# Kernel tuning notes

Measured on AMD Instinct MI355X. Metric: run time of the kernel, lower is better.

## Reference

```python
import jax, jax.numpy as jnp
import numpy as np

D_MODEL = 1024
HEADS = 16
D_K = D_MODEL // HEADS
D_FF = 4096
B, S = 4, 2048
EPS = 1e-5


def _layer_norm(x, gamma, beta):
    mu = jnp.mean(x, axis=-1, keepdims=True)
    var = jnp.mean(jnp.square(x - mu), axis=-1, keepdims=True)
    return (x - mu) * jax.lax.rsqrt(var + EPS) * gamma + beta


def setup_inputs() -> dict:
    key = jax.random.key(0)
    ks = jax.random.split(key, 16)
    s_in = 1.0 / np.sqrt(D_MODEL)
    s_ff = 1.0 / np.sqrt(D_FF)
    inp = {
        "x": jax.random.normal(ks[0], (B, S, D_MODEL), dtype=jnp.float32),
        "src_mask": jnp.ones((B, 1, 1, S), dtype=jnp.int32),
        "Wq": jax.random.uniform(ks[1], (D_MODEL, D_MODEL), jnp.float32, -s_in, s_in),
        "bq": jnp.zeros((D_MODEL,), jnp.float32),
        "Wk": jax.random.uniform(ks[2], (D_MODEL, D_MODEL), jnp.float32, -s_in, s_in),
        "bk": jnp.zeros((D_MODEL,), jnp.float32),
        "Wv": jax.random.uniform(ks[3], (D_MODEL, D_MODEL), jnp.float32, -s_in, s_in),
        "bv": jnp.zeros((D_MODEL,), jnp.float32),
        "Wo": jax.random.uniform(ks[4], (D_MODEL, D_MODEL), jnp.float32, -s_in, s_in),
        "bo": jnp.zeros((D_MODEL,), jnp.float32),
        "W1": jax.random.uniform(ks[5], (D_MODEL, D_FF), jnp.float32, -s_in, s_in),
        "b1": jnp.zeros((D_FF,), jnp.float32),
        "W2": jax.random.uniform(ks[6], (D_FF, D_MODEL), jnp.float32, -s_ff, s_ff),
        "b2": jnp.zeros((D_MODEL,), jnp.float32),
        "g1": jnp.ones((D_MODEL,), jnp.float32),
        "be1": jnp.zeros((D_MODEL,), jnp.float32),
        "g2": jnp.ones((D_MODEL,), jnp.float32),
        "be2": jnp.zeros((D_MODEL,), jnp.float32),
    }
    return inp


def reference(x, src_mask, Wq, bq, Wk, bk, Wv, bv, Wo, bo, W1, b1, W2, b2, g1, be1, g2, be2):
    Bn, L, _ = x.shape
    # Self-attention (dropout=0 / eval)
    q = (x @ Wq + bq).reshape(Bn, L, HEADS, D_K).transpose(0, 2, 1, 3)  # [B,H,L,dk]
    k = (x @ Wk + bk).reshape(Bn, L, HEADS, D_K).transpose(0, 2, 1, 3)
    v = (x @ Wv + bv).reshape(Bn, L, HEADS, D_K).transpose(0, 2, 1, 3)
    scores = jnp.einsum("bhqd,bhkd->bhqk", q, k) / np.sqrt(D_K).astype(np.float32)
    scores = jnp.where(src_mask == 0, -jnp.inf, scores)
    attn = jax.nn.softmax(scores, axis=-1)
    out = jnp.einsum("bhqk,bhkd->bhqd", attn, v)
    out = out.transpose(0, 2, 1, 3).reshape(Bn, L, D_MODEL)
    attn_out = out @ Wo + bo
    x = _layer_norm(x + attn_out, g1, be1)
    # FFN
    ffn = jax.nn.relu(x @ W1 + b1) @ W2 + b2
    x = _layer_norm(x + ffn, g2, be2)
    return x
```

## Files before the change

### kernel.cpp

```cpp
#include <hip/hip_runtime.h>
#include <hip/hip_bf16.h>
#include <cstdint>
#include <cstddef>

typedef __bf16 bf16;
typedef __bf16 bf16x8 __attribute__((ext_vector_type(8)));
typedef float  f32x4  __attribute__((ext_vector_type(4)));
typedef unsigned short u16x4 __attribute__((ext_vector_type(4)));
typedef uint32_t u32x4 __attribute__((ext_vector_type(4)));

static constexpr int D_MODEL = 1024;
static constexpr int HEADS   = 16;
static constexpr int D_KH    = 64;
static constexpr int D_FF    = 4096;
static constexpr int BATCH   = 4;
static constexpr int SEQ     = 2048;
static constexpr int MROWS   = BATCH * SEQ;
static constexpr float QSCALE = 0.18033688011f;

#define VMCNT(n) asm volatile("s_waitcnt vmcnt(" #n ")" ::: "memory")
#define LGKM0()                                            \
  do {                                                     \
    asm volatile("s_waitcnt lgkmcnt(0)" ::: "memory");     \
    __builtin_amdgcn_sched_barrier(0);                     \
  } while (0)

__device__ __forceinline__ unsigned short bfbits(float f) {
  return __builtin_bit_cast(unsigned short, (bf16)f);
}
__device__ __forceinline__ float bf2f(unsigned short u) {
  return __builtin_bit_cast(float, (uint32_t)u << 16);
}

__device__ __forceinline__ void gload_lds16(const void* g, void* l) {
  __builtin_amdgcn_global_load_lds(
      (__attribute__((address_space(1))) uint32_t*)(uintptr_t)g,
      (__attribute__((address_space(3))) uint32_t*)(uintptr_t)l, 16, 0, 0);
}

__global__ void k_cast_mask(const float* __restrict__ in, bf16* __restrict__ out,
                            const int* __restrict__ mask, uint32_t* __restrict__ flags) {
  if (blockIdx.x == 4096) {
    __shared__ uint32_t sb[4];
    int tid = threadIdx.x;
    if (tid < 4) sb[tid] = 0;
    __syncthreads();
    if (tid < 128) {
      int b = tid >> 5, t = tid & 31;
      const int4* p = (const int4*)(mask + b * SEQ + t * 64);
      int all = 1;
#pragma unroll
      for (int i = 0; i < 16; ++i) {
        int4 v = p[i];
        all &= v.x & v.y & v.z & v.w;
      }
      if (all) atomicOr(&sb[b], 1u << t);
    }
    __syncthreads();
    if (tid < 4) flags[tid] = sb[tid];
    return;
  }
  int i = (blockIdx.x * 256 + threadIdx.x) * 8;
  const float4* p = (const float4*)(in + i);
  float4 a = p[0], b = p[1];
  bf16x8 v;
  v[0] = (bf16)a.x; v[1] = (bf16)a.y; v[2] = (bf16)a.z; v[3] = (bf16)a.w;
  v[4] = (bf16)b.x; v[5] = (bf16)b.y; v[6] = (bf16)b.z; v[7] = (bf16)b.w;
  *(bf16x8*)(out + i) = v;
}

struct TPAll {
  const float* w1; const float* w2; const float* wx[4];
  bf16* w1t; bf16* w2t; bf16* wxt[4];
};
__global__ void k_transpose_all(TPAll p) {
  __shared__ float tile[64][65];
  const float* W;
  bf16* Wt;
  int K, N, k0, n0;
  int t = blockIdx.x;
  if (t < 1024) {
    W = p.w1; Wt = p.w1t; K = 1024; N = 4096;
    k0 = (t & 15) * 64; n0 = (t >> 4) * 64;
  } else if (t < 2048) {
    int u = t - 1024;
    W = p.w2; Wt = p.w2t; K = 4096; N = 1024;
    k0 = (u & 63) * 64; n0 = (u >> 6) * 64;
  } else {
    int u = t - 2048;
    int which = u >> 8, v = u & 255;
    W = p.wx[which]; Wt = p.wxt[which]; K = 1024; N = 1024;
    k0 = (v & 15) * 64; n0 = (v >> 4) * 64;
  }
  int c = threadIdx.x & 63, r0 = threadIdx.x >> 6;
#pragma unroll
  for (int i = 0; i < 16; ++i) {
    int r = r0 + i * 4;
    tile[r][c] = W[(size_t)(k0 + r) * N + n0 + c];
  }
  __syncthreads();
#pragma unroll
  for (int i = 0; i < 16; ++i) {
    int r = r0 + i * 4;
    Wt[(size_t)(n0 + r) * K + k0 + c] = (bf16)tile[c][r];
  }
}

enum { EP_RELU = 0, EP_O16 = 1, EP_QKV = 2 };

template <int EPI, int NREP>
__global__ __launch_bounds__(512, 2) void k_gemm8(
    const bf16* __restrict__ A, const bf16* __restrict__ Bt,
    const float* __restrict__ bias, const float* __restrict__ bias2,
    const float* __restrict__ bias3,
    void* __restrict__ Cout, void* __restrict__ C2, void* __restrict__ C3,
    int N, int K) {
  extern __shared__ char smem[];
  constexpr int BN = NREP * 64;
  constexpr int HB = NREP / 2;
  const int tid = threadIdx.x;
  const int lane = tid & 63;
  const int wid = tid >> 6;
  const int wm = wid >> 2, wn = wid & 3;
  const int l15 = lane & 15, l4 = lane >> 4;
  const int bx = blockIdx.x, by = blockIdx.y;
  const int NI = K >> 7;

  const int c0 = tid, c1 = tid + 512;
  const bf16* baseA0 = A + (size_t)(bx * 256 + (c0 >> 3)) * K + ((c0 & 7) ^ ((c0 >> 3) & 7)) * 8;
  const bf16* baseA1 = A + (size_t)(bx * 256 + (c1 >> 3)) * K + ((c1 & 7) ^ ((c1 >> 3) & 7)) * 8;
  const bf16* baseB0 = Bt + (size_t)(by * BN + (c0 >> 3)) * K + ((c0 & 7) ^ ((c0 >> 3) & 7)) * 8;
  const bf16* baseB1 = Bt + (size_t)(by * BN + (c1 >> 3)) * K + ((c1 & 7) ^ ((c1 >> 3) & 7)) * 8;
  const size_t rowK128 = (size_t)128 * K;

  auto stA = [&](int h, int t, int buf) {
    gload_lds16(baseA0 + h * rowK128 + t * 64, smem + buf * 32768 + h * 16384 + c0 * 16);
    gload_lds16(baseA1 + h * rowK128 + t * 64, smem + buf * 32768 + h * 16384 + c1 * 16);
  };
  auto stB = [&](int h, int t, int buf) {
    gload_lds16(baseB0 + h * rowK128 + t * 64,
                smem + 65536 + buf * (HB * 16384) + h * 16384 + c0 * 16);
    gload_lds16(baseB1 + h * rowK128 + t * 64,
                smem + 65536 + buf * (HB * 16384) + h * 16384 + c1 * 16);
  };

  const int ch0 = (l4 ^ (l15 & 7)) * 16;
  const int ch1 = ((4 + l4) ^ (l15 & 7)) * 16;
  const int aoff = l15 * 128;
  int boffh[NREP];
#pragma unroll
  for (int n = 0; n < NREP; ++n) {
    int rB = wn * (NREP * 16) + n * 16 + l15;
    boffh[n] = (rB >> 7) * 16384 + (rB & 127) * 128;
  }

  f32x4 acc[8][NREP] = {};
  bf16x8 breg[NREP][2];

  stA(0, 0, 0); stA(1, 0, 0); stB(0, 0, 0);
  if constexpr (HB == 2) stB(1, 0, 0);
  stA(0, 1, 1); stA(1, 1, 1); stB(0, 1, 1);
  if constexpr (HB == 2) stB(1, 1, 1);

  for (int i = 0; i < NI; ++i) {
    const int t1 = 2 * i + 1, t2 = 2 * i + 2;
    const bool notfirst = (i > 0), notlast = (i + 1 < NI);
#pragma unroll
    for (int p = 0; p < 8; ++p) {
      const int q = p & 3;
      const char* Ab = smem + (p >> 2) * 32768 + wm * 16384;
      const char* Bb = smem + 65536 + (p >> 2) * (HB * 16384);
      if (p == 0) {
        if (notfirst) {
          stA(0, t1, 1);
          VMCNT(2);
        } else {
          if constexpr (HB == 2) VMCNT(8); else VMCNT(6);
        }
        __builtin_amdgcn_s_barrier();
      } else if (p == 4) {
        if (notlast) {
          stA(0, t2, 0);
          VMCNT(2);
        } else {
          VMCNT(0);
        }
        __builtin_amdgcn_s_barrier();
      }
      if (q == 0) {
#pragma unroll
        for (int n = 0; n < NREP; ++n) {
          breg[n][0] = *(const bf16x8*)(Bb + boffh[n] + ch0);
          breg[n][1] = *(const bf16x8*)(Bb + boffh[n] + ch1);
        }
      }
      bf16x8 a0k0 = *(const bf16x8*)(Ab + (2 * q + 0) * 2048 + aoff + ch0);
      bf16x8 a0k1 = *(const bf16x8*)(Ab + (2 * q + 0) * 2048 + aoff + ch1);
      bf16x8 a1k0 = *(const bf16x8*)(Ab + (2 * q + 1) * 2048 + aoff + ch0);
      bf16x8 a1k1 = *(const bf16x8*)(Ab + (2 * q + 1) * 2048 + aoff + ch1);
      if (p == 1) { if (notfirst) stA(1, t1, 1); }
      else if (p == 2) { if (notfirst) stB(0, t1, 1); }
      else if (p == 3) { if constexpr (HB == 2) { if (notfirst) stB(1, t1, 1); } }
      else if (p == 5) { if (notlast) stA(1, t2, 0); }
      else if (p == 6) { if (notlast) stB(0, t2, 0); }
      else if (p == 7) { if constexpr (HB == 2) { if (notlast) stB(1, t2, 0); } }
      if (p != 0 && p != 4) __builtin_amdgcn_s_barrier();
      LGKM0();
      __builtin_amdgcn_s_setprio(1);
#pragma unroll
      for (int n = 0; n < NREP; ++n) {
        acc[2 * q + 0][n] = __builtin_amdgcn_mfma_f32_16x16x32_bf16(a0k0, breg[n][0], acc[2 * q + 0][n], 0, 0, 0);
        acc[2 * q + 0][n] = __builtin_amdgcn_mfma_f32_16x16x32_bf16(a0k1, breg[n][1], acc[2 * q + 0][n], 0, 0, 0);
        acc[2 * q + 1][n] = __builtin_amdgcn_mfma_f32_16x16x32_bf16(a1k0, breg[n][0], acc[2 * q + 1][n], 0, 0, 0);
        acc[2 * q + 1][n] = __builtin_amdgcn_mfma_f32_16x16x32_bf16(a1k1, breg[n][1], acc[2 * q + 1][n], 0, 0, 0);
      }
      __builtin_amdgcn_s_setprio(0);
      __builtin_amdgcn_s_barrier();
    }
  }

  float bia[NREP];
#pragma unroll
  for (int n = 0; n < NREP; ++n) {
    int colL = wn * (NREP * 16) + n * 16 + l15;
    if constexpr (EPI == EP_QKV) {
      const int g = by >> 2;
      const float* bp = (g == 0) ? bias : (g == 1 ? bias2 : bias3);
      bia[n] = bp[(by & 3) * 256 + colL];
    } else {
      bia[n] = bias[by * BN + colL];
    }
  }
#pragma unroll
  for (int mf = 0; mf < 8; ++mf) {
    int row0 = bx * 256 + wm * 128 + mf * 16 + l4 * 4;
#pragma unroll
    for (int n = 0; n < NREP; ++n) {
      int colL = wn * (NREP * 16) + n * 16 + l15;
      if constexpr (EPI == EP_QKV) {
        const int g = by >> 2;
        int cc = (by & 3) * 256 + colL;
        if (g == 2) {
          int bidx = row0 >> 11, s0 = row0 & 2047;
          u16x4 pk;
#pragma unroll
          for (int r = 0; r < 4; ++r) pk[r] = bfbits(acc[mf][n][r] + bia[n]);
          *(u16x4*)((bf16*)C3 + (((size_t)bidx * HEADS + (cc >> 6)) * D_KH + (cc & 63)) * SEQ + s0) = pk;
        } else if (g == 0) {
          bf16* dst = (bf16*)Cout;
#pragma unroll
          for (int r = 0; r < 4; ++r)
            dst[(size_t)(row0 + r) * 1024 + cc] = (bf16)((acc[mf][n][r] + bia[n]) * QSCALE);
        } else {
          bf16* dst = (bf16*)C2;
#pragma unroll
          for (int r = 0; r < 4; ++r)
            dst[(size_t)(row0 + r) * 1024 + cc] = (bf16)(acc[mf][n][r] + bia[n]);
        }
      } else {
        int col = by * BN + colL;
#pragma unroll
        for (int r = 0; r < 4; ++r) {
          float v = acc[mf][n][r] + bia[n];
          if constexpr (EPI == EP_RELU) v = fmaxf(v, 0.f);
          ((bf16*)Cout)[(size_t)(row0 + r) * N + col] = (bf16)v;
        }
      }
    }
  }
}

__global__ __launch_bounds__(256, 4) void k_attn(
    const bf16* __restrict__ Q, const bf16* __restrict__ Kb,
    const bf16* __restrict__ Vt, const int* __restrict__ mask,
    const uint32_t* __restrict__ Mf, bf16* __restrict__ O) {
  __shared__ bf16 Ks[2][64 * 64];
  __shared__ bf16 Vs[2][64 * 64];
  const int tid = threadIdx.x;
  const int lane = tid & 63;
  const int l15 = lane & 15, l4 = lane >> 4;
  const int L = blockIdx.x;
  const int xcd = L & 7, rest = L >> 3;
  const int qx = rest & 15, yhi = rest >> 4;
  const int bh = yhi * 8 + xcd;
  const int b = bh >> 4, h = bh & 15;
  const size_t qrow0 = (size_t)b * SEQ + qx * 128 + (tid >> 6) * 32;
  const bf16* Kbase = Kb + (size_t)b * SEQ * D_MODEL + h * 64;
  const bf16* Vbase = Vt + (size_t)bh * D_KH * SEQ;
  const int* mbase = mask + b * SEQ;
  const uint32_t mflags = Mf[b];

  bf16x8 qf[2][2];
#pragma unroll
  for (int m = 0; m < 2; ++m)
#pragma unroll
    for (int ks = 0; ks < 2; ++ks)
      qf[m][ks] = *(const bf16x8*)&Q[(qrow0 + m * 16 + l15) * D_MODEL + h * 64 + ks * 32 + l4 * 8];

  f32x4 o[2][4] = {};
  f32x4 rs[2] = {};
  bf16x8 ones;
#pragma unroll
  for (int i = 0; i < 8; ++i) ones[i] = (bf16)1.0f;

  auto stage = [&](int buf, int kv0) {
#pragma unroll
    for (int i = 0; i < 2; ++i) {
      int o_ = tid + i * 256;
      int row = o_ >> 3;
      int ch = (o_ & 7) ^ (row & 7);
      gload_lds16(Kbase + (size_t)(kv0 + row) * D_MODEL + ch * 8,
                  (char*)&Ks[buf][0] + o_ * 16);
      gload_lds16(Vbase + (size_t)row * SEQ + kv0 + ch * 8,
                  (char*)&Vs[buf][0] + o_ * 16);
    }
  };

  stage(0, 0);
  __syncthreads();

  for (int kv0 = 0; kv0 < SEQ; kv0 += 64) {
    const int cur = (kv0 >> 6) & 1;
    if (kv0 + 64 < SEQ) stage(cur ^ 1, kv0 + 64);
    const bf16* Kc = &Ks[cur][0];
    const bf16* Vc = &Vs[cur][0];

    f32x4 sf[2][4] = {};
    __builtin_amdgcn_s_setprio(1);
#pragma unroll
    for (int ks = 0; ks < 2; ++ks)
#pragma unroll
      for (int n = 0; n < 4; ++n) {
        int r = n * 16 + l15;
        bf16x8 kf = *(const bf16x8*)&Kc[r * 64 + ((ks * 32 + l4 * 8) ^ ((r & 7) << 3))];
#pragma unroll
        for (int m = 0; m < 2; ++m)
          sf[m][n] = __builtin_amdgcn_mfma_f32_16x16x32_bf16(kf, qf[m][ks], sf[m][n], 0, 0, 0);
      }
    __builtin_amdgcn_s_setprio(0);

    if (__builtin_expect(!((mflags >> (kv0 >> 6)) & 1), 0)) {
#pragma unroll
      for (int n = 0; n < 4; ++n) {
        int4 mk = *(const int4*)&mbase[kv0 + n * 16 + l4 * 4];
#pragma unroll
        for (int r = 0; r < 4; ++r)
          if (((const int*)&mk)[r] == 0) {
            sf[0][n][r] = -1e30f;
            sf[1][n][r] = -1e30f;
          }
      }
    }

    uint32_t pk[2][4][2];
#pragma unroll
    for (int m = 0; m < 2; ++m) {
#pragma unroll
      for (int n = 0; n < 4; ++n) {
#pragma unroll
        for (int r = 0; r < 4; ++r) sf[m][n][r] = exp2f(sf[m][n][r]);
        asm("v_cvt_pk_bf16_f32 %0, %1, %2"
            : "=v"(pk[m][n][0]) : "v"(sf[m][n][0]), "v"(sf[m][n][1]));
        asm("v_cvt_pk_bf16_f32 %0, %1, %2"
            : "=v"(pk[m][n][1]) : "v"(sf[m][n][2]), "v"(sf[m][n][3]));
      }
    }

    bf16x8 pa[2][2];
#pragma unroll
    for (int m = 0; m < 2; ++m)
#pragma unroll
      for (int ks = 0; ks < 2; ++ks) {
        u32x4 w;
#pragma unroll
        for (int hh = 0; hh < 2; ++hh) {
          uint32_t a = pk[m][ks * 2 + 0][hh];
          uint32_t bsw = pk[m][ks * 2 + 1][hh];
          asm("v_permlane32_swap_b32 %0, %1" : "+v"(a), "+v"(bsw));
          asm("v_permlane16_swap_b32 %0, %1" : "+v"(a), "+v"(bsw));
          w[hh] = a;
          w[2 + hh] = bsw;
        }
        pa[ks][m] = __builtin_bit_cast(bf16x8, w);
      }

#pragma unroll
    for (int ks = 0; ks < 2; ++ks) {
      __builtin_amdgcn_s_setprio(1);
#pragma unroll
      for (int n = 0; n < 4; ++n) {
        int d = n * 16 + l15;
        bf16x8 vf = *(const bf16x8*)&Vc[d * 64 + ((ks * 32 + l4 * 8) ^ ((d & 7) << 3))];
#pragma unroll
        for (int m = 0; m < 2; ++m)
          o[m][n] = __builtin_amdgcn_mfma_f32_16x16x32_bf16(pa[ks][m], vf, o[m][n], 0, 0, 0);
      }
#pragma unroll
      for (int m = 0; m < 2; ++m)
        rs[m] = __builtin_amdgcn_mfma_f32_16x16x32_bf16(pa[ks][m], ones, rs[m], 0, 0, 0);
      __builtin_amdgcn_s_setprio(0);
    }
    __syncthreads();
  }

#pragma unroll
  for (int m = 0; m < 2; ++m) {
    float inv[4];
#pragma unroll
    for (int r = 0; r < 4; ++r) inv[r] = 1.0f / rs[m][r];
#pragma unroll
    for (int n = 0; n < 4; ++n)
#pragma unroll
      for (int r = 0; r < 4; ++r)
        O[(qrow0 + m * 16 + l4 * 4 + r) * D_MODEL + h * 64 + n * 16 + l15] =
            (bf16)(o[m][n][r] * inv[r]);
  }
}

__global__ __launch_bounds__(256) void k_add_ln1(
    const float* __restrict__ a, const bf16* __restrict__ b,
    const float* __restrict__ g, const float* __restrict__ be,
    bf16* __restrict__ y) {
  const int t = threadIdx.x;
  const size_t base = (size_t)blockIdx.x * D_MODEL + t * 4;
  float4 va = *(const float4*)(a + base);
  u16x4 vb = *(const u16x4*)(b + base);
  float v0 = va.x + bf2f(vb[0]), v1 = va.y + bf2f(vb[1]);
  float v2 = va.z + bf2f(vb[2]), v3 = va.w + bf2f(vb[3]);
  float s  = v0 + v1 + v2 + v3;
  float s2 = v0 * v0 + v1 * v1 + v2 * v2 + v3 * v3;
#pragma unroll
  for (int off = 1; off < 64; off <<= 1) {
    s  += __shfl_xor(s, off);
    s2 += __shfl_xor(s2, off);
  }
  __shared__ float red1[4], red2[4];
  int w = t >> 6;
  if ((t & 63) == 0) { red1[w] = s; red2[w] = s2; }
  __syncthreads();
  s  = red1[0] + red1[1] + red1[2] + red1[3];
  s2 = red2[0] + red2[1] + red2[2] + red2[3];
  float mu  = s * (1.f / D_MODEL);
  float var = s2 * (1.f / D_MODEL) - mu * mu;
  float rstd = rsqrtf(var + 1e-5f);
  float4 vg  = *(const float4*)(g + t * 4);
  float4 vbe = *(const float4*)(be + t * 4);
  u16x4 pk = {bfbits((v0 - mu) * rstd * vg.x + vbe.x),
              bfbits((v1 - mu) * rstd * vg.y + vbe.y),
              bfbits((v2 - mu) * rstd * vg.z + vbe.z),
              bfbits((v3 - mu) * rstd * vg.w + vbe.w)};
  *(u16x4*)(y + base) = pk;
}

__global__ __launch_bounds__(256) void k_add_ln2(
    const bf16* __restrict__ a, const bf16* __restrict__ b,
    const float* __restrict__ g, const float* __restrict__ be,
    float* __restrict__ y) {
  const int t = threadIdx.x;
  const size_t base = (size_t)blockIdx.x * D_MODEL + t * 4;
  u16x4 va = *(const u16x4*)(a + base);
  u16x4 vb = *(const u16x4*)(b + base);
  float v0 = bf2f(va[0]) + bf2f(vb[0]), v1 = bf2f(va[1]) + bf2f(vb[1]);
  float v2 = bf2f(va[2]) + bf2f(vb[2]), v3 = bf2f(va[3]) + bf2f(vb[3]);
  float s  = v0 + v1 + v2 + v3;
  float s2 = v0 * v0 + v1 * v1 + v2 * v2 + v3 * v3;
#pragma unroll
  for (int off = 1; off < 64; off <<= 1) {
    s  += __shfl_xor(s, off);
    s2 += __shfl_xor(s2, off);
  }
  __shared__ float red1[4], red2[4];
  int w = t >> 6;
  if ((t & 63) == 0) { red1[w] = s; red2[w] = s2; }
  __syncthreads();
  s  = red1[0] + red1[1] + red1[2] + red1[3];
  s2 = red2[0] + red2[1] + red2[2] + red2[3];
  float mu  = s * (1.f / D_MODEL);
  float var = s2 * (1.f / D_MODEL) - mu * mu;
  float rstd = rsqrtf(var + 1e-5f);
  float4 vg  = *(const float4*)(g + t * 4);
  float4 vbe = *(const float4*)(be + t * 4);
  *(float4*)(y + base) = make_float4((v0 - mu) * rstd * vg.x + vbe.x,
                                     (v1 - mu) * rstd * vg.y + vbe.y,
                                     (v2 - mu) * rstd * vg.z + vbe.z,
                                     (v3 - mu) * rstd * vg.w + vbe.w);
}

extern "C" void kernel_launch(void* const* d_in, const int* in_sizes, int n_in,
                              void* d_out, int out_size, void* d_ws, size_t ws_size,
                              hipStream_t stream) {
  const float* x   = (const float*)d_in[0];
  const int*  mask = (const int*)d_in[1];
  const float* Wq  = (const float*)d_in[2];
  const float* bq  = (const float*)d_in[3];
  const float* Wk  = (const float*)d_in[4];
  const float* bk_ = (const float*)d_in[5];
  const float* Wv  = (const float*)d_in[6];
  const float* bv  = (const float*)d_in[7];
  const float* Wo  = (const float*)d_in[8];
  const float* bo  = (const float*)d_in[9];
  const float* W1  = (const float*)d_in[10];
  const float* b1  = (const float*)d_in[11];
  const float* W2  = (const float*)d_in[12];
  const float* b2  = (const float*)d_in[13];
  const float* g1  = (const float*)d_in[14];
  const float* be1 = (const float*)d_in[15];
  const float* g2  = (const float*)d_in[16];
  const float* be2 = (const float*)d_in[17];

  char* ws = (char*)d_ws;
  const size_t MB = 1ull << 20;
  bf16*  xb    = (bf16*)(ws + 0);
  bf16*  Qb    = (bf16*)(ws + 16 * MB);
  bf16*  Kbuf  = (bf16*)(ws + 32 * MB);
  bf16*  Vt    = (bf16*)(ws + 48 * MB);
  bf16*  Hb    = (bf16*)(ws + 0);
  bf16*  aproj = (bf16*)(ws + 64 * MB);
  bf16*  f2o   = (bf16*)(ws + 80 * MB);
  uint32_t* mfl = (uint32_t*)(ws + 96 * MB);
  bf16*  x1b   = (bf16*)(ws + 128 * MB);
  bf16*  Wqkvt = (bf16*)(ws + 144 * MB);
  bf16*  Wot   = (bf16*)(ws + 150 * MB);
  bf16*  W1t   = (bf16*)(ws + 152 * MB);
  bf16*  W2t   = (bf16*)(ws + 160 * MB);
  bf16*  Ob    = xb;

  const int SM4 = 131072, SM2 = 98304;
  hipFuncSetAttribute(reinterpret_cast<const void*>(&k_gemm8<EP_QKV, 4>),
                      hipFuncAttributeMaxDynamicSharedMemorySize, SM4);
  hipFuncSetAttribute(reinterpret_cast<const void*>(&k_gemm8<EP_RELU, 4>),
                      hipFuncAttributeMaxDynamicSharedMemorySize, SM4);
  hipFuncSetAttribute(reinterpret_cast<const void*>(&k_gemm8<EP_O16, 2>),
                      hipFuncAttributeMaxDynamicSharedMemorySize, SM2);

  k_cast_mask<<<4097, 256, 0, stream>>>(x, xb, mask, mfl);
  TPAll tp;
  tp.w1 = W1; tp.w1t = W1t;
  tp.w2 = W2; tp.w2t = W2t;
  tp.wx[0] = Wq; tp.wxt[0] = Wqkvt;
  tp.wx[1] = Wk; tp.wxt[1] = Wqkvt + 1024 * 1024;
  tp.wx[2] = Wv; tp.wxt[2] = Wqkvt + 2 * 1024 * 1024;
  tp.wx[3] = Wo; tp.wxt[3] = Wot;
  k_transpose_all<<<3072, 256, 0, stream>>>(tp);

  k_gemm8<EP_QKV, 4><<<dim3(32, 12), 512, SM4, stream>>>(
      xb, Wqkvt, bq, bk_, bv, Qb, Kbuf, Vt, 3072, 1024);

  k_attn<<<1024, 256, 0, stream>>>(Qb, Kbuf, Vt, mask, mfl, Ob);

  k_gemm8<EP_O16, 2><<<dim3(32, 8), 512, SM2, stream>>>(
      Ob, Wot, bo, nullptr, nullptr, aproj, nullptr, nullptr, 1024, 1024);
  k_add_ln1<<<MROWS, 256, 0, stream>>>(x, aproj, g1, be1, x1b);

  k_gemm8<EP_RELU, 4><<<dim3(32, 16), 512, SM4, stream>>>(
      x1b, W1t, b1, nullptr, nullptr, Hb, nullptr, nullptr, 4096, 1024);
  k_gemm8<EP_O16, 2><<<dim3(32, 8), 512, SM2, stream>>>(
      Hb, W2t, b2, nullptr, nullptr, f2o, nullptr, nullptr, 1024, 4096);
  k_add_ln2<<<MROWS, 256, 0, stream>>>(x1b, f2o, g2, be2, (float*)d_out);
}
```

Baseline: 359.4 us.

## Merge prep kernels, narrow QKV GEMM tiles, hoist attention LDS offsets, read bf16 residual

```diff
diff --git a/kernel.cpp b/kernel.cpp
--- a/kernel.cpp
+++ b/kernel.cpp
@@ -38,59 +38,61 @@
       (__attribute__((address_space(3))) uint32_t*)(uintptr_t)l, 16, 0, 0);
 }
 
-__global__ void k_cast_mask(const float* __restrict__ in, bf16* __restrict__ out,
-                            const int* __restrict__ mask, uint32_t* __restrict__ flags) {
-  if (blockIdx.x == 4096) {
+struct PrepArgs {
+  const float* x; bf16* xb;
+  const int* mask; uint32_t* flags;
+  const float* w1; const float* w2; const float* wx[4];
+  bf16* w1t; bf16* w2t; bf16* wxt[4];
+};
+__global__ void k_prep(PrepArgs p) {
+  __shared__ float tile[64][65];
+  const int t = blockIdx.x;
+  if (t < 4096) {
+    int i = (t * 256 + threadIdx.x) * 8;
+    const float4* q = (const float4*)(p.x + i);
+    float4 a = q[0], b = q[1];
+    bf16x8 v;
+    v[0] = (bf16)a.x; v[1] = (bf16)a.y; v[2] = (bf16)a.z; v[3] = (bf16)a.w;
+    v[4] = (bf16)b.x; v[5] = (bf16)b.y; v[6] = (bf16)b.z; v[7] = (bf16)b.w;
+    *(bf16x8*)(p.xb + i) = v;
+    return;
+  }
+  if (t == 4096) {
     __shared__ uint32_t sb[4];
     int tid = threadIdx.x;
     if (tid < 4) sb[tid] = 0;
     __syncthreads();
     if (tid < 128) {
-      int b = tid >> 5, t = tid & 31;
-      const int4* p = (const int4*)(mask + b * SEQ + t * 64);
+      int b = tid >> 5, tt = tid & 31;
+      const int4* q = (const int4*)(p.mask + b * SEQ + tt * 64);
       int all = 1;
 #pragma unroll
       for (int i = 0; i < 16; ++i) {
-        int4 v = p[i];
+        int4 v = q[i];
         all &= v.x & v.y & v.z & v.w;
       }
-      if (all) atomicOr(&sb[b], 1u << t);
+      if (all) atomicOr(&sb[b], 1u << tt);
     }
     __syncthreads();
-    if (tid < 4) flags[tid] = sb[tid];
+    if (tid < 4) p.flags[tid] = sb[tid];
     return;
   }
-  int i = (blockIdx.x * 256 + threadIdx.x) * 8;
-  const float4* p = (const float4*)(in + i);
-  float4 a = p[0], b = p[1];
-  bf16x8 v;
-  v[0] = (bf16)a.x; v[1] = (bf16)a.y; v[2] = (bf16)a.z; v[3] = (bf16)a.w;
-  v[4] = (bf16)b.x; v[5] = (bf16)b.y; v[6] = (bf16)b.z; v[7] = (bf16)b.w;
-  *(bf16x8*)(out + i) = v;
-}
-
-struct TPAll {
-  const float* w1; const float* w2; const float* wx[4];
-  bf16* w1t; bf16* w2t; bf16* wxt[4];
-};
-__global__ void k_transpose_all(TPAll p) {
-  __shared__ float tile[64][65];
+  int u = t - 4097;
   const float* W;
   bf16* Wt;
   int K, N, k0, n0;
-  int t = blockIdx.x;
-  if (t < 1024) {
+  if (u < 1024) {
     W = p.w1; Wt = p.w1t; K = 1024; N = 4096;
-    k0 = (t & 15) * 64; n0 = (t >> 4) * 64;
-  } else if (t < 2048) {
-    int u = t - 1024;
+    k0 = (u & 15) * 64; n0 = (u >> 4) * 64;
+  } else if (u < 2048) {
+    int v = u - 1024;
     W = p.w2; Wt = p.w2t; K = 4096; N = 1024;
-    k0 = (u & 63) * 64; n0 = (u >> 6) * 64;
+    k0 = (v & 63) * 64; n0 = (v >> 6) * 64;
   } else {
-    int u = t - 2048;
-    int which = u >> 8, v = u & 255;
+    int v = u - 2048;
+    int which = v >> 8, vv = v & 255;
     W = p.wx[which]; Wt = p.wxt[which]; K = 1024; N = 1024;
-    k0 = (v & 15) * 64; n0 = (v >> 4) * 64;
+    k0 = (vv & 15) * 64; n0 = (vv >> 4) * 64;
   }
   int c = threadIdx.x & 63, r0 = threadIdx.x >> 6;
 #pragma unroll
@@ -219,14 +221,15 @@
     }
   }
 
+  constexpr int BPM = 1024 / BN;
   float bia[NREP];
 #pragma unroll
   for (int n = 0; n < NREP; ++n) {
     int colL = wn * (NREP * 16) + n * 16 + l15;
     if constexpr (EPI == EP_QKV) {
-      const int g = by >> 2;
+      const int g = by / BPM;
       const float* bp = (g == 0) ? bias : (g == 1 ? bias2 : bias3);
-      bia[n] = bp[(by & 3) * 256 + colL];
+      bia[n] = bp[(by % BPM) * BN + colL];
     } else {
       bia[n] = bias[by * BN + colL];
     }
@@ -238,8 +241,8 @@
     for (int n = 0; n < NREP; ++n) {
       int colL = wn * (NREP * 16) + n * 16 + l15;
       if constexpr (EPI == EP_QKV) {
-        const int g = by >> 2;
-        int cc = (by & 3) * 256 + colL;
+        const int g = by / BPM;
+        int cc = (by % BPM) * BN + colL;
         if (g == 2) {
           int bidx = row0 >> 11, s0 = row0 & 2047;
           u16x4 pk;
@@ -303,6 +306,9 @@
 #pragma unroll
   for (int i = 0; i < 8; ++i) ones[i] = (bf16)1.0f;
 
+  const int koff0 = l15 * 64 + ((l4 * 8) ^ ((l15 & 7) << 3));
+  const int koff1 = l15 * 64 + ((32 + l4 * 8) ^ ((l15 & 7) << 3));
+
   auto stage = [&](int buf, int kv0) {
 #pragma unroll
     for (int i = 0; i < 2; ++i) {
@@ -331,8 +337,7 @@
     for (int ks = 0; ks < 2; ++ks)
 #pragma unroll
       for (int n = 0; n < 4; ++n) {
-        int r = n * 16 + l15;
-        bf16x8 kf = *(const bf16x8*)&Kc[r * 64 + ((ks * 32 + l4 * 8) ^ ((r & 7) << 3))];
+        bf16x8 kf = *(const bf16x8*)&Kc[(ks ? koff1 : koff0) + n * 1024];
 #pragma unroll
         for (int m = 0; m < 2; ++m)
           sf[m][n] = __builtin_amdgcn_mfma_f32_16x16x32_bf16(kf, qf[m][ks], sf[m][n], 0, 0, 0);
@@ -389,8 +394,7 @@
       __builtin_amdgcn_s_setprio(1);
 #pragma unroll
       for (int n = 0; n < 4; ++n) {
-        int d = n * 16 + l15;
-        bf16x8 vf = *(const bf16x8*)&Vc[d * 64 + ((ks * 32 + l4 * 8) ^ ((d & 7) << 3))];
+        bf16x8 vf = *(const bf16x8*)&Vc[(ks ? koff1 : koff0) + n * 1024];
 #pragma unroll
         for (int m = 0; m < 2; ++m)
           o[m][n] = __builtin_amdgcn_mfma_f32_16x16x32_bf16(pa[ks][m], vf, o[m][n], 0, 0, 0);
@@ -418,15 +422,15 @@
 }
 
 __global__ __launch_bounds__(256) void k_add_ln1(
-    const float* __restrict__ a, const bf16* __restrict__ b,
+    const bf16* __restrict__ a, const bf16* __restrict__ b,
     const float* __restrict__ g, const float* __restrict__ be,
     bf16* __restrict__ y) {
   const int t = threadIdx.x;
   const size_t base = (size_t)blockIdx.x * D_MODEL + t * 4;
-  float4 va = *(const float4*)(a + base);
+  u16x4 va = *(const u16x4*)(a + base);
   u16x4 vb = *(const u16x4*)(b + base);
-  float v0 = va.x + bf2f(vb[0]), v1 = va.y + bf2f(vb[1]);
-  float v2 = va.z + bf2f(vb[2]), v3 = va.w + bf2f(vb[3]);
+  float v0 = bf2f(va[0]) + bf2f(vb[0]), v1 = bf2f(va[1]) + bf2f(vb[1]);
+  float v2 = bf2f(va[2]) + bf2f(vb[2]), v3 = bf2f(va[3]) + bf2f(vb[3]);
   float s  = v0 + v1 + v2 + v3;
   float s2 = v0 * v0 + v1 * v1 + v2 * v2 + v3 * v3;
 #pragma unroll
@@ -517,40 +521,40 @@
   bf16*  Hb    = (bf16*)(ws + 0);
   bf16*  aproj = (bf16*)(ws + 64 * MB);
   bf16*  f2o   = (bf16*)(ws + 80 * MB);
-  uint32_t* mfl = (uint32_t*)(ws + 96 * MB);
+  bf16*  Ob    = (bf16*)(ws + 96 * MB);
+  uint32_t* mfl = (uint32_t*)(ws + 112 * MB);
   bf16*  x1b   = (bf16*)(ws + 128 * MB);
   bf16*  Wqkvt = (bf16*)(ws + 144 * MB);
   bf16*  Wot   = (bf16*)(ws + 150 * MB);
   bf16*  W1t   = (bf16*)(ws + 152 * MB);
   bf16*  W2t   = (bf16*)(ws + 160 * MB);
-  bf16*  Ob    = xb;
 
   const int SM4 = 131072, SM2 = 98304;
-  hipFuncSetAttribute(reinterpret_cast<const void*>(&k_gemm8<EP_QKV, 4>),
-                      hipFuncAttributeMaxDynamicSharedMemorySize, SM4);
+  hipFuncSetAttribute(reinterpret_cast<const void*>(&k_gemm8<EP_QKV, 2>),
+                      hipFuncAttributeMaxDynamicSharedMemorySize, SM2);
   hipFuncSetAttribute(reinterpret_cast<const void*>(&k_gemm8<EP_RELU, 4>),
                       hipFuncAttributeMaxDynamicSharedMemorySize, SM4);
   hipFuncSetAttribute(reinterpret_cast<const void*>(&k_gemm8<EP_O16, 2>),
                       hipFuncAttributeMaxDynamicSharedMemorySize, SM2);
 
-  k_cast_mask<<<4097, 256, 0, stream>>>(x, xb, mask, mfl);
-  TPAll tp;
-  tp.w1 = W1; tp.w1t = W1t;
-  tp.w2 = W2; tp.w2t = W2t;
-  tp.wx[0] = Wq; tp.wxt[0] = Wqkvt;
-  tp.wx[1] = Wk; tp.wxt[1] = Wqkvt + 1024 * 1024;
-  tp.wx[2] = Wv; tp.wxt[2] = Wqkvt + 2 * 1024 * 1024;
-  tp.wx[3] = Wo; tp.wxt[3] = Wot;
-  k_transpose_all<<<3072, 256, 0, stream>>>(tp);
-
-  k_gemm8<EP_QKV, 4><<<dim3(32, 12), 512, SM4, stream>>>(
+  PrepArgs pp;
+  pp.x = x; pp.xb = xb; pp.mask = mask; pp.flags = mfl;
+  pp.w1 = W1; pp.w1t = W1t;
+  pp.w2 = W2; pp.w2t = W2t;
+  pp.wx[0] = Wq; pp.wxt[0] = Wqkvt;
+  pp.wx[1] = Wk; pp.wxt[1] = Wqkvt + 1024 * 1024;
+  pp.wx[2] = Wv; pp.wxt[2] = Wqkvt + 2 * 1024 * 1024;
+  pp.wx[3] = Wo; pp.wxt[3] = Wot;
+  k_prep<<<7169, 256, 0, stream>>>(pp);
+
+  k_gemm8<EP_QKV, 2><<<dim3(32, 24), 512, SM2, stream>>>(
       xb, Wqkvt, bq, bk_, bv, Qb, Kbuf, Vt, 3072, 1024);
 
   k_attn<<<1024, 256, 0, stream>>>(Qb, Kbuf, Vt, mask, mfl, Ob);
 
   k_gemm8<EP_O16, 2><<<dim3(32, 8), 512, SM2, stream>>>(
       Ob, Wot, bo, nullptr, nullptr, aproj, nullptr, nullptr, 1024, 1024);
-  k_add_ln1<<<MROWS, 256, 0, stream>>>(x, aproj, g1, be1, x1b);
+  k_add_ln1<<<MROWS, 256, 0, stream>>>(xb, aproj, g1, be1, x1b);
 
   k_gemm8<EP_RELU, 4><<<dim3(32, 16), 512, SM4, stream>>>(
       x1b, W1t, b1, nullptr, nullptr, Hb, nullptr, nullptr, 4096, 1024);
```

Measured after the change: 352.3 us. 2.0% less time.
